# Optimization experiments

Hardware: AMD Instinct MI355X
Metric: run time of the kernel (lower is better)

Reference implementation:

```python
import jax, jax.numpy as jnp
import numpy as np

N_O = 50000
N_Q = 50000
E = 1_600_000
POS_DIM = 3
LATENT = 128
HEADS = 4
HEAD_DIM = 32
EDGE_IN = 3 * POS_DIM  # ['rel','q_pos','o_pos']


def setup_inputs() -> dict:
    key = jax.random.key(0)
    ks = jax.random.split(key, 12)
    h_obs = jax.random.normal(ks[0], (N_O, LATENT), dtype=jnp.float32)
    pos_obs = jax.random.uniform(ks[1], (N_O, POS_DIM), dtype=jnp.float32)
    pos_query = jax.random.uniform(ks[2], (N_Q, POS_DIM), dtype=jnp.float32)
    src = jax.random.randint(ks[3], (E,), 0, N_O, dtype=jnp.int32)
    dst = jnp.sort(jax.random.randint(ks[4], (E,), 0, N_Q, dtype=jnp.int32))
    s = 0.05
    W1 = jax.random.normal(ks[5], (EDGE_IN, LATENT), dtype=jnp.float32) * s
    b1 = jnp.zeros((LATENT,), dtype=jnp.float32)
    W2 = jax.random.normal(ks[6], (LATENT, HEADS), dtype=jnp.float32) * s
    b2 = jnp.zeros((HEADS,), dtype=jnp.float32)
    Wv = jax.random.normal(ks[7], (LATENT, HEADS * HEAD_DIM), dtype=jnp.float32) * s
    bv = jnp.zeros((HEADS * HEAD_DIM,), dtype=jnp.float32)
    log_sigma = jnp.float32(-2.0)
    return {"h_obs": h_obs, "pos_obs": pos_obs, "pos_query": pos_query,
            "src": src, "dst": dst,
            "W1": W1, "b1": b1, "W2": W2, "b2": b2,
            "Wv": Wv, "bv": bv, "log_sigma": log_sigma}


def _forward(h_obs, pos_obs, pos_query, src, dst, W1, b1, W2, b2, Wv, bv, log_sigma):
    pos_o = pos_obs[src]                      # [E, P]
    pos_q = pos_query[dst]                    # [E, P]
    rel = pos_q - pos_o
    edge_attr = jnp.concatenate([rel, pos_q, pos_o], axis=-1)   # [E, 3P]
    hid = jax.nn.relu(edge_attr @ W1 + b1)                      # [E, LATENT]
    logits = hid @ W2 + b2                                      # [E, H]
    dist2 = jnp.sum(rel * rel, axis=-1, keepdims=True)          # [E, 1]
    sigma = jnp.exp(log_sigma) + 1e-6
    logits = logits - dist2 / (2.0 * sigma * sigma)             # kernel log-weight
    # segment softmax over edges grouped by dst
    n_q = pos_query.shape[0]
    m = jax.ops.segment_max(logits, dst, num_segments=n_q)      # [N_q, H]
    ex = jnp.exp(logits - m[dst])
    denom = jax.ops.segment_sum(ex, dst, num_segments=n_q)      # [N_q, H]
    attn = ex / (denom[dst] + 1e-16)                            # [E, H]
    v = (h_obs @ Wv + bv).reshape(-1, HEADS, HEAD_DIM)          # [N_o, H, D]
    msg = attn[:, :, None] * v[src]                             # [E, H, D]
    out = jax.ops.segment_sum(msg, dst, num_segments=n_q)       # [N_q, H, D]
    return out.reshape(n_q, HEADS * HEAD_DIM)


def reference(h_obs, pos_obs, pos_query, src, dst, W1, b1, W2, b2, Wv, bv, log_sigma):
    return _forward(h_obs, pos_obs, pos_query, src, dst, W1, b1, W2, b2, Wv, bv, log_sigma)
```

## Files before the change

### kernel.cpp

```cpp
#include <hip/hip_runtime.h>
#include <hip/hip_bf16.h>
#include <cstdint>
#include <cstddef>

#define N_O 50000
#define N_Q 50000
#define NE  1600000

#define EDGE_BLOCKS  (NE / 128)
#define VP_BLOCKS    ((N_O + 31) / 32)
#define RP_BLOCKS    ((N_Q + 128) / 128)
#define WCAP 264

#define WVP_OFF   38608768u
#define WVP_BYTES 65536u

typedef __attribute__((ext_vector_type(8)))  short short8;
typedef __attribute__((ext_vector_type(16))) float f32x16;

__device__ inline unsigned short f2bf(float x) {
    __hip_bfloat16 hb = __float2bfloat16(x);
    return *reinterpret_cast<unsigned short*>(&hb);
}

__device__ inline unsigned pk2(float a, float b) {
    __hip_bfloat162 t = __float22bfloat162_rn(make_float2(a, b));
    return *reinterpret_cast<unsigned*>(&t);
}

__global__ void pack_kernel(const float* __restrict__ W1, const float* __restrict__ b1,
                            const float* __restrict__ W2, const float* __restrict__ b2,
                            const float* __restrict__ log_sigma,
                            const float* __restrict__ Wv,
                            unsigned short* __restrict__ W1cT,
                            unsigned short* __restrict__ W2tb,
                            float* __restrict__ scal,
                            unsigned short* __restrict__ WvPhi,
                            unsigned short* __restrict__ WvPlo,
                            int vp_mfma) {
    int j = threadIdx.x;
    if (blockIdx.x == 0) {
        if (j < 128) {
            #pragma unroll
            for (int a = 0; a < 3; ++a) {
                W1cT[j * 8 + a]     = f2bf(W1[(3 + a) * 128 + j] + W1[a * 128 + j]);
                W1cT[j * 8 + 3 + a] = f2bf(W1[(6 + a) * 128 + j] - W1[a * 128 + j]);
            }
            W1cT[j * 8 + 6] = f2bf(b1[j]);
            W1cT[j * 8 + 7] = 0;
            #pragma unroll
            for (int hd = 0; hd < 4; ++hd)
                W2tb[hd * 128 + j] = f2bf(W2[j * 4 + hd]);
        } else if (j == 128) {
            float sigma = expf(log_sigma[0]) + 1e-6f;
            scal[0] = 1.0f / (2.0f * sigma * sigma);
            scal[1] = b2[0]; scal[2] = b2[1]; scal[3] = b2[2]; scal[4] = b2[3];
        }
    } else if (vp_mfma) {
        int fr = (blockIdx.x - 1) * 256 + j;
        int lane = fr & 63, i = lane & 31, g = lane >> 5;
        int ks = (fr >> 6) & 7, c = fr >> 9;
        #pragma unroll
        for (int e = 0; e < 8; ++e) {
            float w = Wv[(size_t)(16 * ks + 8 * g + e) * 128 + 32 * c + i];
            unsigned short hi = f2bf(w);
            float rem = w - __uint_as_float(((unsigned)hi) << 16);
            WvPhi[fr * 8 + e] = hi;
            WvPlo[fr * 8 + e] = f2bf(rem);
        }
    }
}

__device__ void rowptr_body(int bid, const int* __restrict__ dst, int* __restrict__ rp) {
    int q = bid * 128 + threadIdx.x;
    if (q > N_Q) return;
    int lo = 0, hi = NE;
    while (lo < hi) {
        int mid = (lo + hi) >> 1;
        if (dst[mid] < q) lo = mid + 1; else hi = mid;
    }
    rp[q] = lo;
}

__device__ void vproj_mfma_body(int tile, const float* __restrict__ h,
                                const unsigned short* __restrict__ WvPhi,
                                const unsigned short* __restrict__ WvPlo,
                                const float* __restrict__ bv,
                                unsigned short* __restrict__ v) {
    int lane = threadIdx.x & 63, wave = threadIdx.x >> 6;
    int i = lane & 31, g = lane >> 5;
    int n = tile * 32 + i;
    bool nok = (n < N_O);
    const float* hrow = h + (size_t)n * 128;

    short8 Bhi[8], Blo[8];
    #pragma unroll
    for (int ks = 0; ks < 8; ++ks) {
        float4 u0 = make_float4(0.f, 0.f, 0.f, 0.f), u1 = u0;
        if (nok) {
            u0 = *(const float4*)(hrow + 16 * ks + 8 * g);
            u1 = *(const float4*)(hrow + 16 * ks + 8 * g + 4);
        }
        float x[8] = {u0.x, u0.y, u0.z, u0.w, u1.x, u1.y, u1.z, u1.w};
        union { unsigned u[4]; short8 s; } ph, pl;
        #pragma unroll
        for (int p = 0; p < 4; ++p) {
            ph.u[p] = pk2(x[2 * p], x[2 * p + 1]);
            float e0 = x[2 * p]     - __uint_as_float(ph.u[p] << 16);
            float e1 = x[2 * p + 1] - __uint_as_float(ph.u[p] & 0xffff0000u);
            pl.u[p] = pk2(e0, e1);
        }
        Bhi[ks] = ph.s; Blo[ks] = pl.s;
    }

    #pragma unroll 1
    for (int cc = 0; cc < 2; ++cc) {
        int c = 2 * wave + cc;
        f32x16 acc;
        #pragma unroll
        for (int k = 0; k < 16; ++k) acc[k] = 0.f;
        #pragma unroll
        for (int ks = 0; ks < 8; ++ks) {
            int fr = (c * 8 + ks) * 64 + lane;
            short8 Ahi = *(const short8*)(WvPhi + fr * 8);
            short8 Alo = *(const short8*)(WvPlo + fr * 8);
            acc = __builtin_amdgcn_mfma_f32_32x32x16_bf16(Ahi, Bhi[ks], acc, 0, 0, 0);
            acc = __builtin_amdgcn_mfma_f32_32x32x16_bf16(Ahi, Blo[ks], acc, 0, 0, 0);
            acc = __builtin_amdgcn_mfma_f32_32x32x16_bf16(Alo, Bhi[ks], acc, 0, 0, 0);
        }
        if (nok) {
            #pragma unroll
            for (int q = 0; q < 4; ++q) {
                int vc = 32 * c + 8 * q + 4 * g;
                float4 bq = *(const float4*)(bv + vc);
                uint2 ov;
                ov.x = pk2(acc[4 * q + 0] + bq.x, acc[4 * q + 1] + bq.y);
                ov.y = pk2(acc[4 * q + 2] + bq.z, acc[4 * q + 3] + bq.w);
                *(uint2*)(v + (size_t)n * 128 + vc) = ov;
            }
        }
    }
}

__device__ void vproj_f32_body(int bid, const float* __restrict__ h,
                               const float* __restrict__ Wv,
                               const float* __restrict__ bv,
                               unsigned short* __restrict__ v,
                               float* Ash ) {
    int t = threadIdx.x;
    int n0 = bid * 32;
    #pragma unroll
    for (int rep = 0; rep < 8; ++rep) {
        int idx = rep * 128 + t;
        int row = idx >> 5, c4 = (idx & 31) * 4;
        float4 val = make_float4(0.f, 0.f, 0.f, 0.f);
        if (n0 + row < N_O) val = *(const float4*)(h + (size_t)(n0 + row) * 128 + c4);
        float* d = &Ash[row * 132 + c4];
        d[0] = val.x; d[1] = val.y; d[2] = val.z; d[3] = val.w;
    }
    __syncthreads();

    int cg = t & 15, rg = t >> 4;
    int c0 = cg * 8, r0 = rg * 4;
    float acc[4][8];
    #pragma unroll
    for (int i = 0; i < 4; ++i)
        #pragma unroll
        for (int j = 0; j < 8; ++j) acc[i][j] = 0.f;

    const float4* Wv4 = (const float4*)Wv;
    for (int k = 0; k < 128; ++k) {
        float4 b0 = Wv4[k * 32 + cg * 2];
        float4 b1v = Wv4[k * 32 + cg * 2 + 1];
        float bb[8] = {b0.x, b0.y, b0.z, b0.w, b1v.x, b1v.y, b1v.z, b1v.w};
        #pragma unroll
        for (int i = 0; i < 4; ++i) {
            float a = Ash[(r0 + i) * 132 + k];
            #pragma unroll
            for (int j = 0; j < 8; ++j) acc[i][j] += a * bb[j];
        }
    }

    float bvv[8];
    #pragma unroll
    for (int j = 0; j < 8; ++j) bvv[j] = bv[c0 + j];
    #pragma unroll
    for (int i = 0; i < 4; ++i) {
        int n = n0 + r0 + i;
        if (n < N_O) {
            uint4 o;
            o.x = pk2(acc[i][0] + bvv[0], acc[i][1] + bvv[1]);
            o.y = pk2(acc[i][2] + bvv[2], acc[i][3] + bvv[3]);
            o.z = pk2(acc[i][4] + bvv[4], acc[i][5] + bvv[5]);
            o.w = pk2(acc[i][6] + bvv[6], acc[i][7] + bvv[7]);
            *(uint4*)(v + (size_t)n * 128 + c0) = o;
        }
    }
}

__device__ void edge_body(int bid, const float* __restrict__ pos_obs,
                          const float* __restrict__ pos_query,
                          const int* __restrict__ src, const int* __restrict__ dst,
                          const unsigned short* __restrict__ W1cT,
                          const unsigned short* __restrict__ W2tb,
                          const float* __restrict__ scal,
                          float* __restrict__ logitsT,
                          unsigned char* smem ) {
    int t = threadIdx.x;
    int wave = t >> 6, lane = t & 63;
    int i = lane & 31, h = lane >> 5;
    unsigned char* myrow = smem + wave * 8448 + i * 264;

    short8 zero8;
    #pragma unroll
    for (int k = 0; k < 8; ++k) zero8[k] = 0;

    int e = bid * 128 + wave * 64 + lane;
    int s = src[e], d = dst[e];
    float pox = pos_obs[s * 3 + 0], poy = pos_obs[s * 3 + 1], poz = pos_obs[s * 3 + 2];
    float pqx = pos_query[d * 3 + 0], pqy = pos_query[d * 3 + 1], pqz = pos_query[d * 3 + 2];
    float rx = pqx - pox, ry = pqy - poy, rz = pqz - poz;
    float dist2 = rx * rx + ry * ry + rz * rz;

    unsigned pk[4];
    pk[0] = pk2(pqx, pqy);
    pk[1] = pk2(pqz, pox);
    pk[2] = pk2(poy, poz);
    pk[3] = 0x00003F80u;

    unsigned pb[4];
    #pragma unroll
    for (int p = 0; p < 4; ++p) pb[p] = (unsigned)__shfl_xor((int)pk[p], 32);

    union { unsigned u[4]; short8 s8; } beaA, beaB;
    #pragma unroll
    for (int p = 0; p < 4; ++p) {
        beaA.u[p] = h ? 0u : pk[p];
        beaB.u[p] = h ? 0u : pb[p];
    }

    short8 a1[4];
    #pragma unroll
    for (int b = 0; b < 4; ++b)
        a1[b] = (h == 0) ? *(const short8*)(W1cT + (32 * b + i) * 8) : zero8;

    short8 a2[8];
    #pragma unroll
    for (int m = 0; m < 8; ++m)
        a2[m] = (i < 4) ? *(const short8*)(W2tb + i * 128 + m * 16 + h * 8) : zero8;

    float headA[4], headB[4];

    #pragma unroll
    for (int set = 0; set < 2; ++set) {
        const short8 bea = set ? beaB.s8 : beaA.s8;

        f32x16 c1[4];
        #pragma unroll
        for (int b = 0; b < 4; ++b) {
            #pragma unroll
            for (int k = 0; k < 16; ++k) c1[b][k] = 0.0f;
            c1[b] = __builtin_amdgcn_mfma_f32_32x32x16_bf16(a1[b], bea, c1[b], 0, 0, 0);
        }

        #pragma unroll
        for (int b = 0; b < 4; ++b) {
            #pragma unroll
            for (int s_ = 0; s_ < 4; ++s_) {
                float x0 = fmaxf(c1[b][4 * s_ + 0], 0.f);
                float x1 = fmaxf(c1[b][4 * s_ + 1], 0.f);
                float x2 = fmaxf(c1[b][4 * s_ + 2], 0.f);
                float x3 = fmaxf(c1[b][4 * s_ + 3], 0.f);
                uint2 w;
                w.x = pk2(x0, x1);
                w.y = pk2(x2, x3);
                *(uint2*)(myrow + 64 * b + 16 * s_ + 8 * h) = w;
            }
        }

        f32x16 cx, cy;
        #pragma unroll
        for (int k = 0; k < 16; ++k) { cx[k] = 0.0f; cy[k] = 0.0f; }
        #pragma unroll
        for (int m = 0; m < 8; m += 2) {
            uint2 lo0 = *(const uint2*)(myrow + 32 * m + 16 * h);
            uint2 hi0 = *(const uint2*)(myrow + 32 * m + 16 * h + 8);
            uint2 lo1 = *(const uint2*)(myrow + 32 * (m + 1) + 16 * h);
            uint2 hi1 = *(const uint2*)(myrow + 32 * (m + 1) + 16 * h + 8);
            union { unsigned int u[4]; short8 s; } b0, b1u;
            b0.u[0] = lo0.x; b0.u[1] = lo0.y; b0.u[2] = hi0.x; b0.u[3] = hi0.y;
            b1u.u[0] = lo1.x; b1u.u[1] = lo1.y; b1u.u[2] = hi1.x; b1u.u[3] = hi1.y;
            cx = __builtin_amdgcn_mfma_f32_32x32x16_bf16(a2[m],     b0.s,  cx, 0, 0, 0);
            cy = __builtin_amdgcn_mfma_f32_32x32x16_bf16(a2[m + 1], b1u.s, cy, 0, 0, 0);
        }
        float* hd = set ? headB : headA;
        #pragma unroll
        for (int r = 0; r < 4; ++r) hd[r] = cx[r] + cy[r];
    }

    float pen = dist2 * scal[0];
    #pragma unroll
    for (int r = 0; r < 4; ++r) {
        float vB = __shfl_xor(headB[r], 32);
        float val = (h ? vB : headA[r]) + scal[1 + r] - pen;
        logitsT[(size_t)r * NE + e] = val;
    }
}

__global__ __launch_bounds__(128, 4) void fused_kernel(
        const float* __restrict__ pos_obs, const float* __restrict__ pos_query,
        const int* __restrict__ src, const int* __restrict__ dst,
        const unsigned short* __restrict__ W1cT,
        const unsigned short* __restrict__ W2tb,
        const float* __restrict__ scal, float* __restrict__ logitsT,
        const float* __restrict__ h_obs, const float* __restrict__ Wv,
        const float* __restrict__ bv, unsigned short* __restrict__ vbuf,
        int* __restrict__ rp,
        const unsigned short* __restrict__ WvPhi,
        const unsigned short* __restrict__ WvPlo,
        int vp_mfma) {
    __shared__ __align__(16) unsigned char smem[16896];
    int b = blockIdx.x;
    if (b < EDGE_BLOCKS) {
        edge_body(b, pos_obs, pos_query, src, dst, W1cT, W2tb, scal, logitsT, smem);
    } else if (b < EDGE_BLOCKS + VP_BLOCKS) {
        int tile = b - EDGE_BLOCKS;
        if (vp_mfma) vproj_mfma_body(tile, h_obs, WvPhi, WvPlo, bv, vbuf);
        else         vproj_f32_body(tile, h_obs, Wv, bv, vbuf, (float*)smem);
    } else {
        rowptr_body(b - EDGE_BLOCKS - VP_BLOCKS, dst, rp);
    }
}

__global__ __launch_bounds__(256) void attn_kernel(const __hip_bfloat162* __restrict__ vb,
                                                   const float* __restrict__ logitsT,
                                                   const int* __restrict__ src,
                                                   const int* __restrict__ rp,
                                                   float* __restrict__ out) {
    __shared__ __align__(16) float wsh[4 * 4 * WCAP];
    int t = threadIdx.x;
    int lane = t & 63, wave = t >> 6;
    int q = blockIdx.x * 4 + wave;
    int s0 = rp[q], s1 = rp[q + 1];
    int cnt = s1 - s0;
    int h = lane >> 4, i = lane & 15;
    const float* lp = logitsT + (size_t)h * NE;

    float m = -INFINITY;
    for (int e = s0 + i; e < s1; e += 16) m = fmaxf(m, lp[e]);
    #pragma unroll
    for (int off = 8; off; off >>= 1) m = fmaxf(m, __shfl_xor(m, off));

    float acc0 = 0.f, acc1 = 0.f, r;

    if (cnt <= 256) {
        int s0a = s0 & ~3;
        float* wpb = wsh + wave * (4 * WCAP) + h * WCAP;
        float sum = 0.f;
        for (int e = s0 + i; e < s1; e += 16) {
            float w = __expf(lp[e] - m);
            wpb[e - s0a] = w;
            sum += w;
        }
        #pragma unroll
        for (int off = 8; off; off >>= 1) sum += __shfl_xor(sum, off);
        r = 1.0f / (sum + 1e-16f);

        int e = s0;
        int e1 = (s0 + 3) & ~3; if (e1 > s1) e1 = s1;
        for (; e < e1; ++e) {
            float w = wpb[e - s0a];
            float2 f = __bfloat1622float2(vb[(size_t)src[e] * 64 + lane]);
            acc0 += w * f.x; acc1 += w * f.y;
        }
        for (; e + 8 <= s1; e += 8) {
            float4 wa = *(const float4*)(wpb + (e - s0a));
            float4 wb = *(const float4*)(wpb + (e - s0a) + 4);
            int4 sa = *(const int4*)(src + e);
            int4 sb = *(const int4*)(src + e + 4);
            float2 f0 = __bfloat1622float2(vb[(size_t)sa.x * 64 + lane]);
            float2 f1 = __bfloat1622float2(vb[(size_t)sa.y * 64 + lane]);
            float2 f2 = __bfloat1622float2(vb[(size_t)sa.z * 64 + lane]);
            float2 f3 = __bfloat1622float2(vb[(size_t)sa.w * 64 + lane]);
            float2 f4 = __bfloat1622float2(vb[(size_t)sb.x * 64 + lane]);
            float2 f5 = __bfloat1622float2(vb[(size_t)sb.y * 64 + lane]);
            float2 f6 = __bfloat1622float2(vb[(size_t)sb.z * 64 + lane]);
            float2 f7 = __bfloat1622float2(vb[(size_t)sb.w * 64 + lane]);
            acc0 += wa.x * f0.x + wa.y * f1.x + wa.z * f2.x + wa.w * f3.x
                  + wb.x * f4.x + wb.y * f5.x + wb.z * f6.x + wb.w * f7.x;
            acc1 += wa.x * f0.y + wa.y * f1.y + wa.z * f2.y + wa.w * f3.y
                  + wb.x * f4.y + wb.y * f5.y + wb.z * f6.y + wb.w * f7.y;
        }
        for (; e + 4 <= s1; e += 4) {
            float4 w4 = *(const float4*)(wpb + (e - s0a));
            int4 s4 = *(const int4*)(src + e);
            float2 f0 = __bfloat1622float2(vb[(size_t)s4.x * 64 + lane]);
            float2 f1 = __bfloat1622float2(vb[(size_t)s4.y * 64 + lane]);
            float2 f2 = __bfloat1622float2(vb[(size_t)s4.z * 64 + lane]);
            float2 f3 = __bfloat1622float2(vb[(size_t)s4.w * 64 + lane]);
            acc0 += w4.x * f0.x + w4.y * f1.x + w4.z * f2.x + w4.w * f3.x;
            acc1 += w4.x * f0.y + w4.y * f1.y + w4.z * f2.y + w4.w * f3.y;
        }
        for (; e < s1; ++e) {
            float w = wpb[e - s0a];
            float2 f = __bfloat1622float2(vb[(size_t)src[e] * 64 + lane]);
            acc0 += w * f.x; acc1 += w * f.y;
        }
    } else {
        float sum = 0.f;
        for (int e = s0 + i; e < s1; e += 16) sum += __expf(lp[e] - m);
        #pragma unroll
        for (int off = 8; off; off >>= 1) sum += __shfl_xor(sum, off);
        r = 1.0f / (sum + 1e-16f);

        int e = s0;
        for (; e < s1 && (e & 3); ++e) {
            float w = __expf(lp[e] - m);
            float2 f = __bfloat1622float2(vb[(size_t)src[e] * 64 + lane]);
            acc0 += w * f.x; acc1 += w * f.y;
        }
        for (; e + 8 <= s1; e += 8) {
            float4 la = *(const float4*)(lp + e);
            float4 lb = *(const float4*)(lp + e + 4);
            int4 sa = *(const int4*)(src + e);
            int4 sb = *(const int4*)(src + e + 4);
            float w0 = __expf(la.x - m), w1 = __expf(la.y - m);
            float w2 = __expf(la.z - m), w3 = __expf(la.w - m);
            float w4 = __expf(lb.x - m), w5 = __expf(lb.y - m);
            float w6 = __expf(lb.z - m), w7 = __expf(lb.w - m);
            float2 f0 = __bfloat1622float2(vb[(size_t)sa.x * 64 + lane]);
            float2 f1 = __bfloat1622float2(vb[(size_t)sa.y * 64 + lane]);
            float2 f2 = __bfloat1622float2(vb[(size_t)sa.z * 64 + lane]);
            float2 f3 = __bfloat1622float2(vb[(size_t)sa.w * 64 + lane]);
            float2 f4 = __bfloat1622float2(vb[(size_t)sb.x * 64 + lane]);
            float2 f5 = __bfloat1622float2(vb[(size_t)sb.y * 64 + lane]);
            float2 f6 = __bfloat1622float2(vb[(size_t)sb.z * 64 + lane]);
            float2 f7 = __bfloat1622float2(vb[(size_t)sb.w * 64 + lane]);
            acc0 += w0 * f0.x + w1 * f1.x + w2 * f2.x + w3 * f3.x
                  + w4 * f4.x + w5 * f5.x + w6 * f6.x + w7 * f7.x;
            acc1 += w0 * f0.y + w1 * f1.y + w2 * f2.y + w3 * f3.y
                  + w4 * f4.y + w5 * f5.y + w6 * f6.y + w7 * f7.y;
        }
        for (; e + 4 <= s1; e += 4) {
            float4 l4 = *(const float4*)(lp + e);
            int4 s4 = *(const int4*)(src + e);
            float w0 = __expf(l4.x - m);
            float w1 = __expf(l4.y - m);
            float w2 = __expf(l4.z - m);
            float w3 = __expf(l4.w - m);
            float2 f0 = __bfloat1622float2(vb[(size_t)s4.x * 64 + lane]);
            float2 f1 = __bfloat1622float2(vb[(size_t)s4.y * 64 + lane]);
            float2 f2 = __bfloat1622float2(vb[(size_t)s4.z * 64 + lane]);
            float2 f3 = __bfloat1622float2(vb[(size_t)s4.w * 64 + lane]);
            acc0 += w0 * f0.x + w1 * f1.x + w2 * f2.x + w3 * f3.x;
            acc1 += w0 * f0.y + w1 * f1.y + w2 * f2.y + w3 * f3.y;
        }
        for (; e < s1; ++e) {
            float w = __expf(lp[e] - m);
            float2 f = __bfloat1622float2(vb[(size_t)src[e] * 64 + lane]);
            acc0 += w * f.x; acc1 += w * f.y;
        }
    }
    *(float2*)(out + (size_t)q * 128 + lane * 2) = make_float2(acc0 * r, acc1 * r);
}

extern "C" void kernel_launch(void* const* d_in, const int* in_sizes, int n_in,
                              void* d_out, int out_size, void* d_ws, size_t ws_size,
                              hipStream_t stream) {
    const float* h_obs     = (const float*)d_in[0];
    const float* pos_obs   = (const float*)d_in[1];
    const float* pos_query = (const float*)d_in[2];
    const int*   src       = (const int*)d_in[3];
    const int*   dst       = (const int*)d_in[4];
    const float* W1        = (const float*)d_in[5];
    const float* b1        = (const float*)d_in[6];
    const float* W2        = (const float*)d_in[7];
    const float* b2        = (const float*)d_in[8];
    const float* Wv        = (const float*)d_in[9];
    const float* bv        = (const float*)d_in[10];
    const float* log_sigma = (const float*)d_in[11];
    float* out = (float*)d_out;

    char* ws = (char*)d_ws;
    int*            rp      = (int*)(ws + 0);
    float*          scal    = (float*)(ws + 200192);
    unsigned short* W1cT    = (unsigned short*)(ws + 200256);
    unsigned short* W2tb    = (unsigned short*)(ws + 202304);
    unsigned short* vbuf    = (unsigned short*)(ws + 208640);
    float*          logitsT = (float*)(ws + 13008768);
    unsigned short* WvPhi   = (unsigned short*)(ws + WVP_OFF);
    unsigned short* WvPlo   = (unsigned short*)(ws + WVP_OFF + 32768);

    int vp_mfma = (ws_size >= (size_t)WVP_OFF + WVP_BYTES) ? 1 : 0;

    hipLaunchKernelGGL(pack_kernel, dim3(9), dim3(256), 0, stream,
                       W1, b1, W2, b2, log_sigma, Wv, W1cT, W2tb, scal,
                       WvPhi, WvPlo, vp_mfma);
    hipLaunchKernelGGL(fused_kernel, dim3(EDGE_BLOCKS + VP_BLOCKS + RP_BLOCKS),
                       dim3(128), 0, stream,
                       pos_obs, pos_query, src, dst, W1cT, W2tb, scal, logitsT,
                       h_obs, Wv, bv, vbuf, rp, WvPhi, WvPlo, vp_mfma);
    hipLaunchKernelGGL(attn_kernel, dim3(N_Q / 4), dim3(256), 0, stream,
                       (const __hip_bfloat162*)vbuf, logitsT, src, rp, out);
}
```

Baseline: 207.8 us.

## Process four edges per wave with 16-byte gathers in segment aggregation

The common small-segment path of the aggregation kernel now splits the wave into four sub-groups of 16 lanes. Each sub-group handles a different edge and each lane gathers 8 bf16 values with one 16-byte load, replacing one 4-byte load per lane per edge. Partial sums are combined across sub-groups with cross-lane shuffles, and two sub-groups write float4 results. This aims to cut the serial per-edge gather latency and the number of memory instructions, at the cost of more shuffles and half the lanes idling at the store. The 8-way unrolled loop in the large-segment path is also removed.

```diff
diff --git a/kernel.cpp b/kernel.cpp
--- a/kernel.cpp
+++ b/kernel.cpp
@@ -351,95 +351,86 @@
     #pragma unroll
     for (int off = 8; off; off >>= 1) m = fmaxf(m, __shfl_xor(m, off));
 
-    float acc0 = 0.f, acc1 = 0.f, r;
-
     if (cnt <= 256) {
-        int s0a = s0 & ~3;
         float* wpb = wsh + wave * (4 * WCAP) + h * WCAP;
         float sum = 0.f;
         for (int e = s0 + i; e < s1; e += 16) {
             float w = __expf(lp[e] - m);
-            wpb[e - s0a] = w;
+            wpb[e - s0] = w;
             sum += w;
         }
         #pragma unroll
         for (int off = 8; off; off >>= 1) sum += __shfl_xor(sum, off);
-        r = 1.0f / (sum + 1e-16f);
-
+        float r = 1.0f / (sum + 1e-16f);
+
+        int sub = lane >> 4, c = lane & 15;
+        int hc = c >> 2;
+        float rh = __shfl(r, hc << 4);
+        const float* wpb2 = wsh + wave * (4 * WCAP) + hc * WCAP;
+        const unsigned char* vb8 = (const unsigned char*)vb;
+        unsigned coff = (unsigned)(c << 4);
+
+        float a0 = 0.f, a1 = 0.f, a2 = 0.f, a3 = 0.f;
+        float a4 = 0.f, a5 = 0.f, a6 = 0.f, a7 = 0.f;
         int e = s0;
-        int e1 = (s0 + 3) & ~3; if (e1 > s1) e1 = s1;
-        for (; e < e1; ++e) {
-            float w = wpb[e - s0a];
-            float2 f = __bfloat1622float2(vb[(size_t)src[e] * 64 + lane]);
-            acc0 += w * f.x; acc1 += w * f.y;
-        }
-        for (; e + 8 <= s1; e += 8) {
-            float4 wa = *(const float4*)(wpb + (e - s0a));
-            float4 wb = *(const float4*)(wpb + (e - s0a) + 4);
-            int4 sa = *(const int4*)(src + e);
-            int4 sb = *(const int4*)(src + e + 4);
-            float2 f0 = __bfloat1622float2(vb[(size_t)sa.x * 64 + lane]);
-            float2 f1 = __bfloat1622float2(vb[(size_t)sa.y * 64 + lane]);
-            float2 f2 = __bfloat1622float2(vb[(size_t)sa.z * 64 + lane]);
-            float2 f3 = __bfloat1622float2(vb[(size_t)sa.w * 64 + lane]);
-            float2 f4 = __bfloat1622float2(vb[(size_t)sb.x * 64 + lane]);
-            float2 f5 = __bfloat1622float2(vb[(size_t)sb.y * 64 + lane]);
-            float2 f6 = __bfloat1622float2(vb[(size_t)sb.z * 64 + lane]);
-            float2 f7 = __bfloat1622float2(vb[(size_t)sb.w * 64 + lane]);
-            acc0 += wa.x * f0.x + wa.y * f1.x + wa.z * f2.x + wa.w * f3.x
-                  + wb.x * f4.x + wb.y * f5.x + wb.z * f6.x + wb.w * f7.x;
-            acc1 += wa.x * f0.y + wa.y * f1.y + wa.z * f2.y + wa.w * f3.y
-                  + wb.x * f4.y + wb.y * f5.y + wb.z * f6.y + wb.w * f7.y;
-        }
         for (; e + 4 <= s1; e += 4) {
-            float4 w4 = *(const float4*)(wpb + (e - s0a));
-            int4 s4 = *(const int4*)(src + e);
-            float2 f0 = __bfloat1622float2(vb[(size_t)s4.x * 64 + lane]);
-            float2 f1 = __bfloat1622float2(vb[(size_t)s4.y * 64 + lane]);
-            float2 f2 = __bfloat1622float2(vb[(size_t)s4.z * 64 + lane]);
-            float2 f3 = __bfloat1622float2(vb[(size_t)s4.w * 64 + lane]);
-            acc0 += w4.x * f0.x + w4.y * f1.x + w4.z * f2.x + w4.w * f3.x;
-            acc1 += w4.x * f0.y + w4.y * f1.y + w4.z * f2.y + w4.w * f3.y;
-        }
-        for (; e < s1; ++e) {
-            float w = wpb[e - s0a];
-            float2 f = __bfloat1622float2(vb[(size_t)src[e] * 64 + lane]);
-            acc0 += w * f.x; acc1 += w * f.y;
+            int es = e + sub;
+            unsigned sidx = (unsigned)src[es];
+            uint4 vv = *(const uint4*)(vb8 + ((sidx << 8) + coff));
+            float w = wpb2[es - s0];
+            a0 += w * __uint_as_float(vv.x << 16);
+            a1 += w * __uint_as_float(vv.x & 0xffff0000u);
+            a2 += w * __uint_as_float(vv.y << 16);
+            a3 += w * __uint_as_float(vv.y & 0xffff0000u);
+            a4 += w * __uint_as_float(vv.z << 16);
+            a5 += w * __uint_as_float(vv.z & 0xffff0000u);
+            a6 += w * __uint_as_float(vv.w << 16);
+            a7 += w * __uint_as_float(vv.w & 0xffff0000u);
+        }
+        int rem = s1 - e;
+        if (sub < rem) {
+            int es = e + sub;
+            unsigned sidx = (unsigned)src[es];
+            uint4 vv = *(const uint4*)(vb8 + ((sidx << 8) + coff));
+            float w = wpb2[es - s0];
+            a0 += w * __uint_as_float(vv.x << 16);
+            a1 += w * __uint_as_float(vv.x & 0xffff0000u);
+            a2 += w * __uint_as_float(vv.y << 16);
+            a3 += w * __uint_as_float(vv.y & 0xffff0000u);
+            a4 += w * __uint_as_float(vv.z << 16);
+            a5 += w * __uint_as_float(vv.z & 0xffff0000u);
+            a6 += w * __uint_as_float(vv.w << 16);
+            a7 += w * __uint_as_float(vv.w & 0xffff0000u);
+        }
+        #pragma unroll
+        for (int off = 16; off <= 32; off <<= 1) {
+            a0 += __shfl_xor(a0, off);
+            a1 += __shfl_xor(a1, off);
+            a2 += __shfl_xor(a2, off);
+            a3 += __shfl_xor(a3, off);
+            a4 += __shfl_xor(a4, off);
+            a5 += __shfl_xor(a5, off);
+            a6 += __shfl_xor(a6, off);
+            a7 += __shfl_xor(a7, off);
+        }
+        if (sub < 2) {
+            float4 o = sub ? make_float4(a4 * rh, a5 * rh, a6 * rh, a7 * rh)
+                           : make_float4(a0 * rh, a1 * rh, a2 * rh, a3 * rh);
+            *(float4*)(out + (size_t)q * 128 + c * 8 + sub * 4) = o;
         }
     } else {
         float sum = 0.f;
         for (int e = s0 + i; e < s1; e += 16) sum += __expf(lp[e] - m);
         #pragma unroll
         for (int off = 8; off; off >>= 1) sum += __shfl_xor(sum, off);
-        r = 1.0f / (sum + 1e-16f);
+        float r = 1.0f / (sum + 1e-16f);
+        float acc0 = 0.f, acc1 = 0.f;
 
         int e = s0;
         for (; e < s1 && (e & 3); ++e) {
             float w = __expf(lp[e] - m);
             float2 f = __bfloat1622float2(vb[(size_t)src[e] * 64 + lane]);
             acc0 += w * f.x; acc1 += w * f.y;
-        }
-        for (; e + 8 <= s1; e += 8) {
-            float4 la = *(const float4*)(lp + e);
-            float4 lb = *(const float4*)(lp + e + 4);
-            int4 sa = *(const int4*)(src + e);
-            int4 sb = *(const int4*)(src + e + 4);
-            float w0 = __expf(la.x - m), w1 = __expf(la.y - m);
-            float w2 = __expf(la.z - m), w3 = __expf(la.w - m);
-            float w4 = __expf(lb.x - m), w5 = __expf(lb.y - m);
-            float w6 = __expf(lb.z - m), w7 = __expf(lb.w - m);
-            float2 f0 = __bfloat1622float2(vb[(size_t)sa.x * 64 + lane]);
-            float2 f1 = __bfloat1622float2(vb[(size_t)sa.y * 64 + lane]);
-            float2 f2 = __bfloat1622float2(vb[(size_t)sa.z * 64 + lane]);
-            float2 f3 = __bfloat1622float2(vb[(size_t)sa.w * 64 + lane]);
-            float2 f4 = __bfloat1622float2(vb[(size_t)sb.x * 64 + lane]);
-            float2 f5 = __bfloat1622float2(vb[(size_t)sb.y * 64 + lane]);
-            float2 f6 = __bfloat1622float2(vb[(size_t)sb.z * 64 + lane]);
-            float2 f7 = __bfloat1622float2(vb[(size_t)sb.w * 64 + lane]);
-            acc0 += w0 * f0.x + w1 * f1.x + w2 * f2.x + w3 * f3.x
-                  + w4 * f4.x + w5 * f5.x + w6 * f6.x + w7 * f7.x;
-            acc1 += w0 * f0.y + w1 * f1.y + w2 * f2.y + w3 * f3.y
-                  + w4 * f4.y + w5 * f5.y + w6 * f6.y + w7 * f7.y;
         }
         for (; e + 4 <= s1; e += 4) {
             float4 l4 = *(const float4*)(lp + e);
@@ -460,8 +451,8 @@
             float2 f = __bfloat1622float2(vb[(size_t)src[e] * 64 + lane]);
             acc0 += w * f.x; acc1 += w * f.y;
         }
-    }
-    *(float2*)(out + (size_t)q * 128 + lane * 2) = make_float2(acc0 * r, acc1 * r);
+        *(float2*)(out + (size_t)q * 128 + lane * 2) = make_float2(acc0 * r, acc1 * r);
+    }
 }
 
 extern "C" void kernel_launch(void* const* d_in, const int* in_sizes, int n_in,
```

Result: slower. 213.6 us (+2.8%).
